# Optimization experiments

Measured on AMD Instinct MI355X. Metric: run time of the kernel, lower is better.

## Reference

```python
import jax, jax.numpy as jnp
import numpy as np

B, T, IN, H, G, O, D = 64, 256, 256, 1024, 256, 64, 4
GO = G + O  # graph_size + out_channels = 320


def _lstm_cell(x, h, c, Wih, Whh, bih, bhh):
    # torch.nn.LSTMCell gate order: i, f, g, o
    g = x @ Wih.T + h @ Whh.T + (bih + bhh)
    i, f, gg, o = jnp.split(g, 4, axis=-1)
    c_new = jax.nn.sigmoid(f) * c + jax.nn.sigmoid(i) * jnp.tanh(gg)
    h_new = jax.nn.sigmoid(o) * jnp.tanh(c_new)
    return h_new, c_new


def _mlp(x, W1, b1, W2, b2, W3, b3):
    # make_mlp with linear_depth=3: Linear->SiLU->Linear->SiLU->Linear
    x = jax.nn.silu(x @ W1.T + b1)
    x = jax.nn.silu(x @ W2.T + b2)
    return x @ W3.T + b3


def setup_inputs() -> dict:
    key = jax.random.key(0)
    ks = iter(jax.random.split(key, 64))
    def p(shape, s=0.05):
        return jax.random.normal(next(ks), shape, jnp.float32) * s
    inp = {}
    inp["z"] = jax.random.normal(next(ks), (B, IN), jnp.float32)
    inp["m_true"] = jax.random.normal(next(ks), (B, T, GO), jnp.float32)
    for pre, od in (("eh", H), ("ec", H), ("ex", O)):
        inp[pre + "_W1"] = p((H, IN)); inp[pre + "_b1"] = p((H,))
        inp[pre + "_W2"] = p((H, H));  inp[pre + "_b2"] = p((H,))
        inp[pre + "_W3"] = p((od, H)); inp[pre + "_b3"] = p((od,))
    inp["in_Wih"] = p((4 * H, GO)); inp["in_Whh"] = p((4 * H, H))
    inp["in_bih"] = p((4 * H,));    inp["in_bhh"] = p((4 * H,))
    inp["rnns_Wih"] = p((D, 4 * H, H)); inp["rnns_Whh"] = p((D, 4 * H, H))
    inp["rnns_bih"] = p((D, 4 * H));    inp["rnns_bhh"] = p((D, 4 * H))
    inp["hA_W"] = p((D, H, H)); inp["hA_b"] = p((D, H))
    inp["cA_W"] = p((D, H, H)); inp["cA_b"] = p((D, H))
    inp["lastH_W"] = p((GO, H)); inp["lastH_b"] = p((GO,))
    inp["lastC_W"] = p((GO, H)); inp["lastC_b"] = p((GO,))
    inp["out_Wih"] = p((4 * GO, H)); inp["out_Whh"] = p((4 * GO, GO))
    inp["out_bih"] = p((4 * GO,));   inp["out_bhh"] = p((4 * GO,))
    return inp


def reference(z, m_true,
              eh_W1, eh_b1, eh_W2, eh_b2, eh_W3, eh_b3,
              ec_W1, ec_b1, ec_W2, ec_b2, ec_W3, ec_b3,
              ex_W1, ex_b1, ex_W2, ex_b2, ex_W3, ex_b3,
              in_Wih, in_Whh, in_bih, in_bhh,
              rnns_Wih, rnns_Whh, rnns_bih, rnns_bhh,
              hA_W, hA_b, cA_W, cA_b,
              lastH_W, lastH_b, lastC_W, lastC_b,
              out_Wih, out_Whh, out_bih, out_bhh):
    h0 = _mlp(z, eh_W1, eh_b1, eh_W2, eh_b2, eh_W3, eh_b3)
    c0 = _mlp(z, ec_W1, ec_b1, ec_W2, ec_b2, ec_W3, ec_b3)
    x_last = _mlp(z, ex_W1, ex_b1, ex_W2, ex_b2, ex_W3, ex_b3)
    m_hat0 = jnp.concatenate(
        [jnp.zeros((z.shape[0], G), z.dtype), x_last], axis=-1)  # [B, GO]
    # flip time, use first T-1 steps; time-major for scan: [T-1, B, GO]
    mt = jnp.flip(m_true, axis=1)[:, :-1, :].transpose(1, 0, 2)

    def step(carry, m_t):
        h0_, c0_ = carry
        h2, c2 = _lstm_cell(m_t, h0_, c0_, in_Wih, in_Whh, in_bih, in_bhh)
        c1 = c2
        for i in range(D):  # recurrent_depth inner chain (fixed, structural)
            h1 = h2 @ hA_W[i].T + hA_b[i]
            c1 = c2 @ cA_W[i].T + cA_b[i]
            h2, c2 = _lstm_cell(h2, h1, c1,
                                rnns_Wih[i], rnns_Whh[i],
                                rnns_bih[i], rnns_bhh[i])
        # note: original reuses c1 (last adapter output) for last_c_adapter
        hh = h2 @ lastH_W.T + lastH_b
        cc = c1 @ lastC_W.T + lastC_b
        ho, _ = _lstm_cell(h2, hh, cc, out_Wih, out_Whh, out_bih, out_bhh)
        return (h2, c2), ho

    _, outs = jax.lax.scan(step, (h0, c0), mt)  # outs: [T-1, B, GO]
    m_hat = jnp.concatenate([m_hat0[:, None, :], outs.transpose(1, 0, 2)],
                            axis=1)  # [B, T, GO]
    return m_hat
```

## Files before the change

### kernel.cpp

```cpp
#include <hip/hip_runtime.h>


typedef unsigned int u32;
typedef unsigned long long u64;
typedef unsigned short u16;
typedef __attribute__((ext_vector_type(8))) __bf16 bf16x8;
typedef __attribute__((ext_vector_type(4))) float f32x4;

#define DEVI __device__ __forceinline__

union FRAG { bf16x8 v; u16 s[8]; u64 q[2]; };
union P4 { u64 q; u16 s[4]; };
union F4 { u64 q[2]; float f[4]; };

DEVI u16 f2bf(float x){ u32 u = __float_as_uint(x); return (u16)((u + 0x7fffu + ((u>>16)&1u)) >> 16); }
DEVI float sigm(float x){ return 1.0f/(1.0f + __expf(-x)); }
DEVI float tanh_(float x){ return 2.0f/(1.0f + __expf(-2.0f*x)) - 1.0f; }
DEVI void ast(void* p, u64 v){ __hip_atomic_store((u64*)p, v, __ATOMIC_RELAXED, __HIP_MEMORY_SCOPE_AGENT); }

#define MFMA16(a,b,c) __builtin_amdgcn_mfma_f32_16x16x32_bf16(a, b, c, 0, 0, 0)

#define NARR 168
#define NWG 169
#define NREP 21
#define NEPOCH 1276

#define SCHEDB() __builtin_amdgcn_sched_barrier(0)
#define WAITV(n) do{ SCHEDB(); \
  asm volatile("s_waitcnt vmcnt(" #n ")" ::: "memory"); \
  SCHEDB(); }while(0)

#if __has_builtin(__builtin_amdgcn_fence)
#define FENCE_ACQ() __builtin_amdgcn_fence(__ATOMIC_ACQUIRE, "agent")
#else
#define FENCE_ACQ() __hip_atomic_fence(__ATOMIC_ACQUIRE, __HIP_MEMORY_SCOPE_AGENT)
#endif

__global__ __launch_bounds__(256, 1) void k_scan(
    const float* __restrict__ m_true,
    const u16* __restrict__ Wcell, const u16* __restrict__ Win_h,
    const u16* __restrict__ Win_x, const u16* __restrict__ Wout,
    const u16* __restrict__ WccA,
    const float* __restrict__ b_in, const float* __restrict__ b_cell,
    const float* __restrict__ cAb, const float* __restrict__ b_out,
    const float* __restrict__ b_cc,
    u16* hS, u16* cS, float* cF, float* ccB, float* outp, u32* bar)
{
  const int wg = blockIdx.x;
  const int tid = threadIdx.x;
  const int wave = tid >> 6, lane = tid & 63;

  if (wg == NARR){
    if (wave == 0){
      u32* arr = bar;
      u32* go  = bar + NARR*32;
      for (u32 ep = 1; ep <= NEPOCH; ++ep){
        for(;;){
          int ok = 1;
          if (lane < 56){
            u32 a0 = __hip_atomic_load(arr + lane*32,       __ATOMIC_RELAXED, __HIP_MEMORY_SCOPE_AGENT);
            u32 a1 = __hip_atomic_load(arr + (lane+56)*32,  __ATOMIC_RELAXED, __HIP_MEMORY_SCOPE_AGENT);
            u32 a2 = __hip_atomic_load(arr + (lane+112)*32, __ATOMIC_RELAXED, __HIP_MEMORY_SCOPE_AGENT);
            ok = (a0 >= ep) && (a1 >= ep) && (a2 >= ep);
          }
          if (__all(ok)) break;
          __builtin_amdgcn_s_sleep(1);
        }
        if (lane < NREP)
          __hip_atomic_store(go + lane*32, ep, __ATOMIC_RELAXED, __HIP_MEMORY_SCOPE_AGENT);
      }
    }
    return;
  }

  int pipe, lw;
  if (wg < 160){ pipe = (wg >> 3) & 1; lw = ((wg >> 4) << 3) | (wg & 7); }
  else         { pipe = (wg - 160) >> 2; lw = 80 + ((wg - 160) & 3); }

  const int bl = lane & 15, kg = lane >> 4;
  const int pair = wave >> 1;
  const int bt = (pipe << 1) + (wave & 1);
  const int b  = (bt << 4) + bl;
  const int swz = (bl & 7) << 4;
  const int foff = ((bl << 2) + kg) << 4;
  const int woff = (bt << 15) + ((lw >> 1) << 10) + (bl << 6) + ((lw & 1) << 5) + (kg << 3);
  __shared__ __align__(16) u16 ldsW[81920];

  auto stage1 = [&](const u16* src, u16* lb, int segs){
    const u16* g = src + (lane << 3);
    u16* l = lb;
    for (int s = 0; s < segs; ++s){
      __builtin_amdgcn_global_load_lds(
          (const __attribute__((address_space(1))) void*)g,
          (__attribute__((address_space(3))) void*)l, 16, 0, 0);
      g += 512; l += 512;
    }
    SCHEDB();
  };
  auto afL = [&](const u16* lb, int row, int kb) -> bf16x8 {
    return *(const bf16x8*)((const char*)lb + row*512 + (kb ^ swz));
  };

  auto gsync = [&](u32 ep, const u16* pfsrc, int cstride, int spw, const u16* xsrc){
    SCHEDB();
    __syncthreads();
    if (tid == 0)
      __hip_atomic_store(bar + wg*32, ep, __ATOMIC_RELAXED, __HIP_MEMORY_SCOPE_AGENT);
    if (wave == 0) FENCE_ACQ();
    SCHEDB();
    if (pfsrc) stage1(pfsrc + (size_t)wave*cstride, ldsW + wave*cstride, spw);
    if (xsrc)  stage1(xsrc + wave*4096, ldsW + 65536 + wave*4096, 8);
    SCHEDB();
    if (tid == 0){
      const u32* gp = bar + NARR*32 + (wg % NREP)*32;
      while (__hip_atomic_load(gp, __ATOMIC_RELAXED, __HIP_MEMORY_SCOPE_AGENT) < ep)
        __builtin_amdgcn_s_sleep(1);
      asm volatile("" ::: "memory");
    }
    __syncthreads();
    SCHEDB();
  };

  auto phase_incell = [&](int t, const u16* hIn, u16* hOut, u16* cOut){
    f32x4 A0={0,0,0,0}, A1={0,0,0,0}, A2={0,0,0,0}, A3={0,0,0,0};
    const char* hf = (const char*)hIn + (bt << 15) + foff;
    const int ksb = pair << 4;
    int jl = (kg << 2), jj = (lw << 4) + jl;
    FRAG sh[2][8], xf[10], pa[8];
    f32x4 bg0, bg1, bg2, bg3, cpv;
    #pragma unroll
    for (int ks = 0; ks < 8; ++ks) sh[0][ks].v = *(const bf16x8*)(hf + (ksb + ks)*1024);
    #pragma unroll
    for (int ks = 0; ks < 8; ++ks) sh[1][ks].v = *(const bf16x8*)(hf + (ksb + 8 + ks)*1024);
    SCHEDB();
    if (wave < 2){
      bg0 = *(const f32x4*)(b_in +        jj);
      bg1 = *(const f32x4*)(b_in + 1024 + jj);
      bg2 = *(const f32x4*)(b_in + 2048 + jj);
      bg3 = *(const f32x4*)(b_in + 3072 + jj);
      cpv = *(const f32x4*)((const char*)cF + ((size_t)b << 12) + (jj << 2));
    } else {
      const float* xr = m_true + (size_t)b*81920 + (size_t)(255 - t)*320;
      #pragma unroll
      for (int ks = 0; ks < 10; ++ks){
        int k = (ks << 5) + (kg << 3);
        f32x4 x0 = *(const f32x4*)(xr + k);
        f32x4 x1 = *(const f32x4*)(xr + k + 4);
        xf[ks].s[0]=f2bf(x0[0]); xf[ks].s[1]=f2bf(x0[1]); xf[ks].s[2]=f2bf(x0[2]); xf[ks].s[3]=f2bf(x0[3]);
        xf[ks].s[4]=f2bf(x1[0]); xf[ks].s[5]=f2bf(x1[1]); xf[ks].s[6]=f2bf(x1[2]); xf[ks].s[7]=f2bf(x1[3]);
      }
      const char* p2 = (const char*)(Win_x + (size_t)lw*20480 + 16384);
      #pragma unroll
      for (int k2 = 0; k2 < 2; ++k2)
        #pragma unroll
        for (int rb = 0; rb < 4; ++rb)
          pa[k2*4+rb].v = *(const bf16x8*)(p2 + (rb*16 + bl)*128 + (((k2<<6)+(kg<<4)) ^ swz));
    }
    SCHEDB();
    WAITV(8);
    const u16* lbA = ldsW + (pair*2)*16384;
    #pragma unroll
    for (int ks = 0; ks < 8; ++ks){
      int kb = (ks << 6) + (kg << 4);
      FRAG a;
      a.v = afL(lbA, bl, kb);      A0 = MFMA16(a.v, sh[0][ks].v, A0);
      a.v = afL(lbA, 16 + bl, kb); A1 = MFMA16(a.v, sh[0][ks].v, A1);
      a.v = afL(lbA, 32 + bl, kb); A2 = MFMA16(a.v, sh[0][ks].v, A2);
      a.v = afL(lbA, 48 + bl, kb); A3 = MFMA16(a.v, sh[0][ks].v, A3);
    }
    WAITV(0);
    const u16* lbB = ldsW + (pair*2+1)*16384;
    #pragma unroll
    for (int ks = 0; ks < 8; ++ks){
      int kb = (ks << 6) + (kg << 4);
      FRAG a;
      a.v = afL(lbB, bl, kb);      A0 = MFMA16(a.v, sh[1][ks].v, A0);
      a.v = afL(lbB, 16 + bl, kb); A1 = MFMA16(a.v, sh[1][ks].v, A1);
      a.v = afL(lbB, 32 + bl, kb); A2 = MFMA16(a.v, sh[1][ks].v, A2);
      a.v = afL(lbB, 48 + bl, kb); A3 = MFMA16(a.v, sh[1][ks].v, A3);
    }
    if (wave >= 2){
      const u16* lb4 = ldsW + 65536;
      #pragma unroll
      for (int ks = 0; ks < 8; ++ks){
        int kb = (ks << 6) + (kg << 4);
        FRAG a;
        a.v = afL(lb4, bl, kb);      A0 = MFMA16(a.v, xf[ks].v, A0);
        a.v = afL(lb4, 16 + bl, kb); A1 = MFMA16(a.v, xf[ks].v, A1);
        a.v = afL(lb4, 32 + bl, kb); A2 = MFMA16(a.v, xf[ks].v, A2);
        a.v = afL(lb4, 48 + bl, kb); A3 = MFMA16(a.v, xf[ks].v, A3);
      }
      #pragma unroll
      for (int k2 = 0; k2 < 2; ++k2){
        A0 = MFMA16(pa[k2*4+0].v, xf[8+k2].v, A0);
        A1 = MFMA16(pa[k2*4+1].v, xf[8+k2].v, A1);
        A2 = MFMA16(pa[k2*4+2].v, xf[8+k2].v, A2);
        A3 = MFMA16(pa[k2*4+3].v, xf[8+k2].v, A3);
      }
    }
    __syncthreads();
    float* red = (float*)ldsW;
    if (wave >= 2){
      float* r = red + ((wave&1)*64 + lane)*20;
      *(f32x4*)(r+0) = A0; *(f32x4*)(r+4) = A1;
      *(f32x4*)(r+8) = A2; *(f32x4*)(r+12) = A3;
    }
    __syncthreads();
    if (wave < 2){
      const float* r = red + ((wave&1)*64 + lane)*20;
      A0 += *(const f32x4*)(r+0); A1 += *(const f32x4*)(r+4);
      A2 += *(const f32x4*)(r+8); A3 += *(const f32x4*)(r+12);
      P4 hw, cw;
      #pragma unroll
      for (int rr = 0; rr < 4; ++rr){
        float gi = A0[rr] + bg0[rr];
        float gf = A1[rr] + bg1[rr];
        float gg = A2[rr] + bg2[rr];
        float go = A3[rr] + bg3[rr];
        float cn = sigm(gf)*cpv[rr] + sigm(gi)*tanh_(gg);
        hw.s[rr] = f2bf(sigm(go)*tanh_(cn));
        cw.s[rr] = f2bf(cn);
      }
      ast((char*)hOut + woff, hw.q);
      ast((char*)cOut + woff, cw.q);
    }
  };

  auto phase_cell = [&](int i, const u16* hIn, const u16* cIn, u16* hOut, u16* cOut, bool last){
    f32x4 A0={0,0,0,0}, A1={0,0,0,0}, A2={0,0,0,0}, A3={0,0,0,0}, A4={0,0,0,0};
    const char* hf  = (const char*)hIn + (bt << 15) + foff;
    const char* cfr = (const char*)cIn + (bt << 15) + foff;
    const int ksb = pair << 4;
    int jl = (kg << 2), jj = (lw << 4) + jl;
    FRAG sh[2][8], sc[2][8];
    f32x4 bg0, bg1, bg2, bg3, bca;
    #pragma unroll
    for (int ks = 0; ks < 8; ++ks){
      sh[0][ks].v = *(const bf16x8*)(hf  + (ksb + ks)*1024);
      sc[0][ks].v = *(const bf16x8*)(cfr + (ksb + ks)*1024);
    }
    #pragma unroll
    for (int ks = 0; ks < 8; ++ks){
      sh[1][ks].v = *(const bf16x8*)(hf  + (ksb + 8 + ks)*1024);
      sc[1][ks].v = *(const bf16x8*)(cfr + (ksb + 8 + ks)*1024);
    }
    SCHEDB();
    if (wave < 2){
      bg0 = *(const f32x4*)(b_cell + i*4096 +        jj);
      bg1 = *(const f32x4*)(b_cell + i*4096 + 1024 + jj);
      bg2 = *(const f32x4*)(b_cell + i*4096 + 2048 + jj);
      bg3 = *(const f32x4*)(b_cell + i*4096 + 3072 + jj);
      bca = *(const f32x4*)(cAb + i*1024 + jj);
    }
    SCHEDB();
    WAITV(16);
    const u16* lbA = ldsW + (pair*2)*20480;
    #pragma unroll
    for (int ks = 0; ks < 8; ++ks){
      int kb = (ks << 6) + (kg << 4);
      FRAG a;
      a.v = afL(lbA, bl, kb);      A0 = MFMA16(a.v, sh[0][ks].v, A0);
      a.v = afL(lbA, 16 + bl, kb); A1 = MFMA16(a.v, sh[0][ks].v, A1);
      a.v = afL(lbA, 32 + bl, kb); A2 = MFMA16(a.v, sh[0][ks].v, A2);
      a.v = afL(lbA, 48 + bl, kb); A3 = MFMA16(a.v, sh[0][ks].v, A3);
      a.v = afL(lbA, 64 + bl, kb); A4 = MFMA16(a.v, sc[0][ks].v, A4);
    }
    WAITV(0);
    const u16* lbB = ldsW + (pair*2+1)*20480;
    #pragma unroll
    for (int ks = 0; ks < 8; ++ks){
      int kb = (ks << 6) + (kg << 4);
      FRAG a;
      a.v = afL(lbB, bl, kb);      A0 = MFMA16(a.v, sh[1][ks].v, A0);
      a.v = afL(lbB, 16 + bl, kb); A1 = MFMA16(a.v, sh[1][ks].v, A1);
      a.v = afL(lbB, 32 + bl, kb); A2 = MFMA16(a.v, sh[1][ks].v, A2);
      a.v = afL(lbB, 48 + bl, kb); A3 = MFMA16(a.v, sh[1][ks].v, A3);
      a.v = afL(lbB, 64 + bl, kb); A4 = MFMA16(a.v, sc[1][ks].v, A4);
    }
    __syncthreads();
    float* red = (float*)ldsW;
    if (wave >= 2){
      float* r = red + ((wave&1)*64 + lane)*20;
      *(f32x4*)(r+0) = A0; *(f32x4*)(r+4) = A1;
      *(f32x4*)(r+8) = A2; *(f32x4*)(r+12) = A3; *(f32x4*)(r+16) = A4;
    }
    __syncthreads();
    if (wave < 2){
      const float* r = red + ((wave&1)*64 + lane)*20;
      A0 += *(const f32x4*)(r+0); A1 += *(const f32x4*)(r+4);
      A2 += *(const f32x4*)(r+8); A3 += *(const f32x4*)(r+12);
      A4 += *(const f32x4*)(r+16);
      P4 hw, cw; F4 cf4;
      #pragma unroll
      for (int rr = 0; rr < 4; ++rr){
        float gi = A0[rr] + bg0[rr];
        float gf = A1[rr] + bg1[rr];
        float gg = A2[rr] + bg2[rr];
        float go = A3[rr] + bg3[rr];
        float c1 = A4[rr] + bca[rr];
        float cn = sigm(gf)*c1 + sigm(gi)*tanh_(gg);
        hw.s[rr] = f2bf(sigm(go)*tanh_(cn));
        cw.s[rr] = f2bf(cn);
        cf4.f[rr] = cn;
      }
      ast((char*)hOut + woff, hw.q);
      ast((char*)cOut + woff, cw.q);
      if (last){
        char* cfp = (char*)cF + ((size_t)b << 12) + (jj << 2);
        ast(cfp, cf4.q[0]); ast(cfp + 8, cf4.q[1]);
      }
    }
  };

  auto phase_ccA = [&](const u16* cIn){
    f32x4 A = {0,0,0,0};
    int w2 = lw - 64;
    const char* cfr = (const char*)cIn + (bt << 15) + foff;
    const int ksb = pair << 4;
    int jl = (kg << 2), jjo = (w2 << 4) + jl;
    FRAG sc[2][8];
    f32x4 bcc;
    #pragma unroll
    for (int ks = 0; ks < 8; ++ks) sc[0][ks].v = *(const bf16x8*)(cfr + (ksb + ks)*1024);
    #pragma unroll
    for (int ks = 0; ks < 8; ++ks) sc[1][ks].v = *(const bf16x8*)(cfr + (ksb + 8 + ks)*1024);
    SCHEDB();
    if (wave < 2) bcc = *(const f32x4*)(b_cc + jjo);
    SCHEDB();
    WAITV(8);
    const u16* lbA = ldsW + (pair*2)*4096;
    #pragma unroll
    for (int ks = 0; ks < 8; ++ks){
      int kb = (ks << 6) + (kg << 4);
      FRAG a; a.v = afL(lbA, bl, kb);
      A = MFMA16(a.v, sc[0][ks].v, A);
    }
    WAITV(0);
    const u16* lbB = ldsW + (pair*2+1)*4096;
    #pragma unroll
    for (int ks = 0; ks < 8; ++ks){
      int kb = (ks << 6) + (kg << 4);
      FRAG a; a.v = afL(lbB, bl, kb);
      A = MFMA16(a.v, sc[1][ks].v, A);
    }
    __syncthreads();
    float* red = (float*)ldsW;
    if (wave >= 2) *(f32x4*)(red + ((wave&1)*64 + lane)*20) = A;
    __syncthreads();
    if (wave < 2){
      A += *(const f32x4*)(red + ((wave&1)*64 + lane)*20);
      F4 v;
      #pragma unroll
      for (int rr = 0; rr < 4; ++rr) v.f[rr] = A[rr] + bcc[rr];
      char* cp2 = (char*)ccB + ((size_t)b*320 + jjo)*4;
      ast(cp2, v.q[0]); ast(cp2 + 8, v.q[1]);
    }
  };

  auto phase_out = [&](int t, const u16* hIn){
    f32x4 A0={0,0,0,0}, A1={0,0,0,0}, A2={0,0,0,0}, A3={0,0,0,0};
    int w2 = lw - 64;
    const char* hf = (const char*)hIn + (bt << 15) + foff;
    const int ksb = pair << 4;
    int jl = (kg << 2), jjo = (w2 << 4) + jl;
    FRAG sh[2][8];
    f32x4 bg0, bg1, bg2, bg3, ccv;
    #pragma unroll
    for (int ks = 0; ks < 8; ++ks) sh[0][ks].v = *(const bf16x8*)(hf + (ksb + ks)*1024);
    #pragma unroll
    for (int ks = 0; ks < 8; ++ks) sh[1][ks].v = *(const bf16x8*)(hf + (ksb + 8 + ks)*1024);
    SCHEDB();
    if (wave < 2){
      bg0 = *(const f32x4*)(b_out +       jjo);
      bg1 = *(const f32x4*)(b_out + 320 + jjo);
      bg2 = *(const f32x4*)(b_out + 640 + jjo);
      bg3 = *(const f32x4*)(b_out + 960 + jjo);
      ccv = *(const f32x4*)((const char*)ccB + ((size_t)b*320 + jjo)*4);
    }
    SCHEDB();
    WAITV(8);
    const u16* lbA = ldsW + (pair*2)*16384;
    #pragma unroll
    for (int ks = 0; ks < 8; ++ks){
      int kb = (ks << 6) + (kg << 4);
      FRAG a;
      a.v = afL(lbA, bl, kb);      A0 = MFMA16(a.v, sh[0][ks].v, A0);
      a.v = afL(lbA, 16 + bl, kb); A1 = MFMA16(a.v, sh[0][ks].v, A1);
      a.v = afL(lbA, 32 + bl, kb); A2 = MFMA16(a.v, sh[0][ks].v, A2);
      a.v = afL(lbA, 48 + bl, kb); A3 = MFMA16(a.v, sh[0][ks].v, A3);
    }
    WAITV(0);
    const u16* lbB = ldsW + (pair*2+1)*16384;
    #pragma unroll
    for (int ks = 0; ks < 8; ++ks){
      int kb = (ks << 6) + (kg << 4);
      FRAG a;
      a.v = afL(lbB, bl, kb);      A0 = MFMA16(a.v, sh[1][ks].v, A0);
      a.v = afL(lbB, 16 + bl, kb); A1 = MFMA16(a.v, sh[1][ks].v, A1);
      a.v = afL(lbB, 32 + bl, kb); A2 = MFMA16(a.v, sh[1][ks].v, A2);
      a.v = afL(lbB, 48 + bl, kb); A3 = MFMA16(a.v, sh[1][ks].v, A3);
    }
    __syncthreads();
    float* red = (float*)ldsW;
    if (wave >= 2){
      float* r = red + ((wave&1)*64 + lane)*20;
      *(f32x4*)(r+0) = A0; *(f32x4*)(r+4) = A1;
      *(f32x4*)(r+8) = A2; *(f32x4*)(r+12) = A3;
    }
    __syncthreads();
    if (wave < 2){
      const float* r = red + ((wave&1)*64 + lane)*20;
      A0 += *(const f32x4*)(r+0); A1 += *(const f32x4*)(r+4);
      A2 += *(const f32x4*)(r+8); A3 += *(const f32x4*)(r+12);
      f32x4 ho;
      #pragma unroll
      for (int rr = 0; rr < 4; ++rr){
        float gi = A0[rr] + bg0[rr];
        float gf = A1[rr] + bg1[rr];
        float gg = A2[rr] + bg2[rr];
        float go = A3[rr] + bg3[rr];
        float cn = sigm(gf)*ccv[rr] + sigm(gi)*tanh_(gg);
        ho[rr] = sigm(go)*tanh_(cn);
      }
      *(f32x4*)(outp + (size_t)b*81920 + (size_t)(t+1)*320 + jjo) = ho;
    }
  };

  if (lw < 64){
    stage1(Win_h + ((size_t)lw << 16) + wave*16384, ldsW + wave*16384, 32);
    stage1(Win_x + (size_t)lw*20480 + wave*4096, ldsW + 65536 + wave*4096, 8);
  }
  __syncthreads();
  SCHEDB();

  u16* hB0 = hS;        u16* hB1 = hS + 65536;
  u16* cB0 = cS;        u16* cB1 = cS + 65536;

  u32 ep = 1;
  if (lw < 64) phase_incell(0, hB1, hB0, cB0);
  gsync(ep++, (lw < 64) ? Wcell + (size_t)lw*81920 : nullptr, 20480, 40, nullptr);
  int p = 1;
  #pragma unroll 1
  for (int t = 0; t < 255; ++t){
    #pragma unroll 1
    for (int i = 0; i < 4; ++i){
      u16* hIn = (p & 1) ? hB0 : hB1;  u16* cIn = (p & 1) ? cB0 : cB1;
      u16* hOut = (p & 1) ? hB1 : hB0; u16* cOut = (p & 1) ? cB1 : cB0;
      if (lw < 64)      phase_cell(i, hIn, cIn, hOut, cOut, i == 3);
      else if (i == 3)  phase_ccA(cIn);
      const u16* pf = nullptr; const u16* xs = nullptr; int cstride = 0, spw = 0;
      if (lw < 64){
        if (i < 3){ pf = Wcell + (size_t)((i+1)*64 + lw)*81920; cstride = 20480; spw = 40; }
        else      { pf = Win_h + ((size_t)lw << 16); cstride = 16384; spw = 32;
                    xs = Win_x + (size_t)lw*20480; }
      } else {
        if (i == 2){ pf = WccA + ((size_t)(lw-64) << 14); cstride = 4096; spw = 8; }
        else if (i == 3){ pf = Wout + ((size_t)(lw-64) << 16); cstride = 16384; spw = 32; }
      }
      gsync(ep++, pf, cstride, spw, xs);
      ++p;
    }
    u16* hIn = (p & 1) ? hB0 : hB1;
    u16* hOut = (p & 1) ? hB1 : hB0; u16* cOut = (p & 1) ? cB1 : cB0;
    if (lw >= 64)       phase_out(t, hIn);
    else if (t < 254)   phase_incell(t + 1, hIn, hOut, cOut);
    gsync(ep++, (lw < 64 && t < 254) ? Wcell + (size_t)lw*81920 : nullptr, 20480, 40, nullptr);
    ++p;
  }
}


__global__ __launch_bounds__(256) void k_dense(const float* __restrict__ X, int xmode,
    const float* __restrict__ W, const float* __restrict__ bias,
    int OD, int ID, int act, int omode, float* outF, u16* outB)
{
  int o = blockIdx.x*4 + (threadIdx.x >> 6);
  if (o >= OD) return;
  int lane = threadIdx.x & 63;
  const float* wr = W + (size_t)o*ID;
  float acc = 0.f;
  if (xmode == 0){ for (int k = 0; k < ID; ++k) acc = fmaf(wr[k], X[(size_t)lane*ID + k], acc); }
  else           { for (int k = 0; k < ID; ++k) acc = fmaf(wr[k], X[(size_t)k*64 + lane], acc); }
  acc += bias[o];
  if (act) acc = acc * sigm(acc);
  if (omode == 0)      outF[(size_t)o*64 + lane] = acc;
  else if (omode == 1){
    int bt = lane >> 4, blx = lane & 15;
    outB[(size_t)bt*16384 + (size_t)(o>>5)*512 + blx*32 + ((o&31)>>3)*8 + (o&7)] = f2bf(acc);
  }
  else if (omode == 2) outF[(size_t)lane*1024 + o] = acc;
  else                 outF[(size_t)lane*81920 + 256 + o] = acc;
}

__global__ void k_zero0(float* out){ out[(size_t)blockIdx.x*81920 + threadIdx.x] = 0.f; }

__global__ __launch_bounds__(256) void k_tr(const float* __restrict__ in, u16* __restrict__ out, int M, int N){
  __shared__ u16 t[64][65];
  int m0 = blockIdx.x << 6, n0 = blockIdx.y << 6;
  int c = threadIdx.x & 63, rq = threadIdx.x >> 6;
  for (int rr = 0; rr < 16; ++rr){
    int r = (rq << 4) + rr;
    t[r][c] = f2bf(in[(size_t)(m0 + r)*N + n0 + c]);
  }
  __syncthreads();
  for (int rr = 0; rr < 16; ++rr){
    int r = (rq << 4) + rr;
    out[(size_t)(n0 + r)*M + m0 + c] = t[c][r];
  }
}

__global__ __launch_bounds__(256) void k_fuse(const float* __restrict__ Whh, const float* __restrict__ Wih,
    const u16* __restrict__ BT, int KM, int mode, u16* __restrict__ dst)
{
  int bx = blockIdx.x, by = blockIdx.y, bz = blockIdx.z;
  int lane = threadIdx.x & 63, wv = threadIdx.x >> 6;
  int bl = lane & 15, kg = lane >> 4;
  int jbase = (mode == 0) ? bz*1024 : ((mode == 1) ? bz*320 : 0);
  int jrow = jbase + bx*16 + bl;
  int k2c = by*64 + wv*16 + bl;
  f32x4 acc = {0,0,0,0};
  for (int m0 = 0; m0 < KM; m0 += 32){
    f32x4 wa0 = *(const f32x4*)(Whh + (size_t)jrow*KM + m0 + (kg << 3));
    f32x4 wa1 = *(const f32x4*)(Whh + (size_t)jrow*KM + m0 + (kg << 3) + 4);
    FRAG a;
    a.s[0]=f2bf(wa0[0]); a.s[1]=f2bf(wa0[1]); a.s[2]=f2bf(wa0[2]); a.s[3]=f2bf(wa0[3]);
    a.s[4]=f2bf(wa1[0]); a.s[5]=f2bf(wa1[1]); a.s[6]=f2bf(wa1[2]); a.s[7]=f2bf(wa1[3]);
    FRAG bb; bb.v = *(const bf16x8*)(BT + (size_t)k2c*KM + m0 + (kg << 3));
    acc = MFMA16(a.v, bb.v, acc);
  }
  #pragma unroll
  for (int r = 0; r < 4; ++r){
    int jl = (kg << 2) + r;
    int jg = jbase + bx*16 + jl;
    float v = acc[r];
    if (mode < 2) v += Wih[(size_t)jg*1024 + k2c];
    int re = (mode == 2) ? jl : (bz*16 + jl);
    int c = k2c >> 8, kl = k2c & 255;
    size_t pos;
    if (mode == 0)      pos = (size_t)bx*81920 + c*20480 + re*256 + (kl ^ ((re&7)<<3));
    else if (mode == 1) pos = (size_t)bx*65536 + c*16384 + re*256 + (kl ^ ((re&7)<<3));
    else                pos = (size_t)bx*16384 + c*4096  + re*256 + (kl ^ ((re&7)<<3));
    dst[pos] = f2bf(v);
  }
}

__global__ void k_pack_winh(const float* __restrict__ src, u16* __restrict__ dst){
  int id = blockIdx.x*256 + threadIdx.x;
  int j = id >> 10, k = id & 1023;
  int g = j >> 10, jj = j & 1023;
  int w = jj >> 4, r = (g << 4) + (jj & 15);
  int c = k >> 8, kl = k & 255;
  dst[(size_t)w*65536 + c*16384 + r*256 + (kl ^ ((r&7)<<3))] = f2bf(src[id]);
}

__global__ void k_pack_winx(const float* __restrict__ src, u16* __restrict__ dst){
  int j = blockIdx.x, k = threadIdx.x;
  int g = j >> 10, jj = j & 1023;
  int w = jj >> 4, r = (g << 4) + (jj & 15);
  float v = src[(size_t)j*320 + k];
  size_t pos;
  if (k < 256) pos = (size_t)w*20480 + r*256 + (k ^ ((r&7)<<3));
  else         pos = (size_t)w*20480 + 16384 + r*64 + ((k - 256) ^ ((r&7)<<3));
  dst[pos] = f2bf(v);
}

__global__ void k_pack_ca(const float* __restrict__ src, u16* __restrict__ dst){
  int id = blockIdx.x*256 + threadIdx.x;
  int jj = id >> 10, k = id & 1023;
  int w = jj >> 4, r = 64 + (jj & 15);
  int c = k >> 8, kl = k & 255;
  dst[(size_t)w*81920 + c*20480 + r*256 + (kl ^ ((r&7)<<3))] = f2bf(src[id]);
}

__global__ __launch_bounds__(256) void k_bias(const float* __restrict__ A, const float* __restrict__ x,
    const float* __restrict__ a1, const float* __restrict__ a2, float* __restrict__ o, int NJ, int K)
{
  int j = blockIdx.x*4 + (threadIdx.x >> 6);
  if (j >= NJ) return;
  int lane = threadIdx.x & 63;
  float acc = 0.f;
  if (A) for (int k = lane; k < K; k += 64) acc += A[(size_t)j*K + k]*x[k];
  for (int off = 32; off; off >>= 1) acc += __shfl_down(acc, off);
  if (lane == 0) o[j] = acc + (a1 ? a1[j] : 0.f) + (a2 ? a2[j] : 0.f);
}

extern "C" void kernel_launch(void* const* d_in, const int* in_sizes, int n_in,
                              void* d_out, int out_size, void* d_ws, size_t ws_size,
                              hipStream_t stream)
{
  (void)in_sizes; (void)n_in; (void)out_size;
  const float* z      = (const float*)d_in[0];
  const float* m_true = (const float*)d_in[1];
  const float* eh_W1=(const float*)d_in[2],  *eh_b1=(const float*)d_in[3];
  const float* eh_W2=(const float*)d_in[4],  *eh_b2=(const float*)d_in[5];
  const float* eh_W3=(const float*)d_in[6],  *eh_b3=(const float*)d_in[7];
  const float* ec_W1=(const float*)d_in[8],  *ec_b1=(const float*)d_in[9];
  const float* ec_W2=(const float*)d_in[10], *ec_b2=(const float*)d_in[11];
  const float* ec_W3=(const float*)d_in[12], *ec_b3=(const float*)d_in[13];
  const float* ex_W1=(const float*)d_in[14], *ex_b1=(const float*)d_in[15];
  const float* ex_W2=(const float*)d_in[16], *ex_b2=(const float*)d_in[17];
  const float* ex_W3=(const float*)d_in[18], *ex_b3=(const float*)d_in[19];
  const float* in_Wih=(const float*)d_in[20], *in_Whh=(const float*)d_in[21];
  const float* in_bih=(const float*)d_in[22], *in_bhh=(const float*)d_in[23];
  const float* r_Wih=(const float*)d_in[24],  *r_Whh=(const float*)d_in[25];
  const float* r_bih=(const float*)d_in[26],  *r_bhh=(const float*)d_in[27];
  const float* hA_W=(const float*)d_in[28],   *hA_b=(const float*)d_in[29];
  const float* cA_W=(const float*)d_in[30],   *cA_b=(const float*)d_in[31];
  const float* lastH_W=(const float*)d_in[32], *lastH_b=(const float*)d_in[33];
  const float* lastC_W=(const float*)d_in[34], *lastC_b=(const float*)d_in[35];
  const float* out_Wih=(const float*)d_in[36], *out_Whh=(const float*)d_in[37];
  const float* out_bih=(const float*)d_in[38], *out_bhh=(const float*)d_in[39];
  float* out = (float*)d_out;

  char* wsb = (char*)d_ws;
  size_t off = 0;
  auto alloc = [&](size_t bytes)->char*{
    char* p = wsb + off; off = (off + bytes + 255) & ~(size_t)255; return p;
  };
  u32* bar    = (u32*)alloc(256*32*4);
  u16* hS     = (u16*)alloc(2*64*1024*2);
  u16* cS     = (u16*)alloc(2*64*1024*2);
  float* cF   = (float*)alloc(64*1024*4);
  float* ccB  = (float*)alloc(64*320*4);
  float* b_in = (float*)alloc(4096*4);
  float* b_cell=(float*)alloc(4*4096*4);
  float* b_out= (float*)alloc(1280*4);
  float* b_cc = (float*)alloc(320*4);
  float* t1   = (float*)alloc(1024*64*4);
  float* t2   = (float*)alloc(1024*64*4);
  u16* Tbuf   = (u16*)alloc((size_t)1024*1024*2);
  u16* Win_h  = (u16*)alloc((size_t)64*65536*2);
  u16* Win_x  = (u16*)alloc((size_t)64*20480*2);
  u16* Wcell  = (u16*)alloc((size_t)4*64*81920*2);
  u16* Wout   = (u16*)alloc((size_t)20*65536*2);
  u16* WccA   = (u16*)alloc((size_t)20*16384*2);
  if (off > ws_size) return;

  hipMemsetAsync(bar, 0, 256*32*4, stream);

  k_dense<<<256,256,0,stream>>>(z, 0, eh_W1, eh_b1, 1024, 256, 1, 0, t1, nullptr);
  k_dense<<<256,256,0,stream>>>(t1,1, eh_W2, eh_b2, 1024,1024, 1, 0, t2, nullptr);
  k_dense<<<256,256,0,stream>>>(t2,1, eh_W3, eh_b3, 1024,1024, 0, 1, nullptr, hS + 65536);
  k_dense<<<256,256,0,stream>>>(z, 0, ec_W1, ec_b1, 1024, 256, 1, 0, t1, nullptr);
  k_dense<<<256,256,0,stream>>>(t1,1, ec_W2, ec_b2, 1024,1024, 1, 0, t2, nullptr);
  k_dense<<<256,256,0,stream>>>(t2,1, ec_W3, ec_b3, 1024,1024, 0, 2, cF, nullptr);
  k_dense<<<256,256,0,stream>>>(z, 0, ex_W1, ex_b1, 1024, 256, 1, 0, t1, nullptr);
  k_dense<<<256,256,0,stream>>>(t1,1, ex_W2, ex_b2, 1024,1024, 1, 0, t2, nullptr);
  k_dense<<<16 ,256,0,stream>>>(t2,1, ex_W3, ex_b3,   64,1024, 0, 3, out, nullptr);
  k_zero0<<<64,256,0,stream>>>(out);

  k_pack_winh<<<16384,256,0,stream>>>(in_Whh, Win_h);
  k_pack_winx<<<4096,320,0,stream>>>(in_Wih, Win_x);
  for (int i = 0; i < 4; ++i)
    k_pack_ca<<<4096,256,0,stream>>>(cA_W + (size_t)i*1024*1024, Wcell + (size_t)i*64*81920);

  for (int i = 0; i < 4; ++i){
    k_tr<<<dim3(16,16),256,0,stream>>>(hA_W + (size_t)i*1024*1024, Tbuf, 1024, 1024);
    k_fuse<<<dim3(64,16,4),256,0,stream>>>(r_Whh + (size_t)i*4096*1024,
                                           r_Wih + (size_t)i*4096*1024,
                                           Tbuf, 1024, 0, Wcell + (size_t)i*64*81920);
  }
  k_tr<<<dim3(5,16),256,0,stream>>>(lastH_W, Tbuf, 320, 1024);
  k_fuse<<<dim3(20,16,4),256,0,stream>>>(out_Whh, out_Wih, Tbuf, 320, 1, Wout);
  k_tr<<<dim3(16,16),256,0,stream>>>(cA_W + (size_t)3*1024*1024, Tbuf, 1024, 1024);
  k_fuse<<<dim3(20,16,1),256,0,stream>>>(lastC_W, nullptr, Tbuf, 1024, 2, WccA);

  k_bias<<<1024,256,0,stream>>>(nullptr, nullptr, in_bih, in_bhh, b_in, 4096, 0);
  for (int i = 0; i < 4; ++i)
    k_bias<<<1024,256,0,stream>>>(r_Whh + (size_t)i*4096*1024, hA_b + i*1024,
                                  r_bih + i*4096, r_bhh + i*4096, b_cell + i*4096, 4096, 1024);
  k_bias<<<320,256,0,stream>>>(out_Whh, lastH_b, out_bih, out_bhh, b_out, 1280, 320);
  k_bias<<<80 ,256,0,stream>>>(lastC_W, cA_b + 3*1024, lastC_b, nullptr, b_cc, 320, 1024);

  k_scan<<<NWG,256,0,stream>>>(m_true, Wcell, Win_h, Win_x, Wout, WccA,
                               b_in, b_cell, cA_b, b_out, b_cc,
                               hS, cS, cF, ccB, out, bar);
}
```

Before: 12.20 ms.

## Replace arbiter-block barrier with per-pipe flag polling and keep cell state in registers

Removes the dedicated arbiter workgroup that gathered arrival flags and broadcast go signals. Each workgroup's wave 0 now polls the arrival flags of its own pipe (84 workgroups) directly, which cuts one hop from every grid barrier. The final cell state and the ccA adapter output are kept in registers across steps instead of round-tripping through global buffers. Loads are issued through inline asm with sc0/sc1 cache-bypass bits and finer vmcnt waits so more memory traffic overlaps the MFMAs. Correctness now depends on the relaxed flag polling plus the cache-bypass loads giving enough memory ordering without an explicit acquire fence.

```diff
diff --git a/kernel.cpp b/kernel.cpp
--- a/kernel.cpp
+++ b/kernel.cpp
@@ -18,23 +18,24 @@
 DEVI float tanh_(float x){ return 2.0f/(1.0f + __expf(-2.0f*x)) - 1.0f; }
 DEVI void ast(void* p, u64 v){ __hip_atomic_store((u64*)p, v, __ATOMIC_RELAXED, __HIP_MEMORY_SCOPE_AGENT); }
 
+DEVI void ld16sc(FRAG& d, const void* p){
+  asm volatile("global_load_dwordx4 %0, %1, off sc0 sc1" : "=v"(d.v) : "v"(p));
+}
+DEVI void ld16(FRAG& d, const void* p){
+  asm volatile("global_load_dwordx4 %0, %1, off" : "=v"(d.v) : "v"(p));
+}
+DEVI void ldf4(f32x4& d, const void* p){
+  asm volatile("global_load_dwordx4 %0, %1, off" : "=v"(d) : "v"(p));
+}
+
 #define MFMA16(a,b,c) __builtin_amdgcn_mfma_f32_16x16x32_bf16(a, b, c, 0, 0, 0)
 
-#define NARR 168
-#define NWG 169
-#define NREP 21
-#define NEPOCH 1276
+#define NWG 168
 
 #define SCHEDB() __builtin_amdgcn_sched_barrier(0)
 #define WAITV(n) do{ SCHEDB(); \
   asm volatile("s_waitcnt vmcnt(" #n ")" ::: "memory"); \
   SCHEDB(); }while(0)
-
-#if __has_builtin(__builtin_amdgcn_fence)
-#define FENCE_ACQ() __builtin_amdgcn_fence(__ATOMIC_ACQUIRE, "agent")
-#else
-#define FENCE_ACQ() __hip_atomic_fence(__ATOMIC_ACQUIRE, __HIP_MEMORY_SCOPE_AGENT)
-#endif
 
 __global__ __launch_bounds__(256, 1) void k_scan(
     const float* __restrict__ m_true,
@@ -44,34 +45,11 @@
     const float* __restrict__ b_in, const float* __restrict__ b_cell,
     const float* __restrict__ cAb, const float* __restrict__ b_out,
     const float* __restrict__ b_cc,
-    u16* hS, u16* cS, float* cF, float* ccB, float* outp, u32* bar)
+    u16* hS, u16* cS, float* cF, float* outp, u32* bar)
 {
   const int wg = blockIdx.x;
   const int tid = threadIdx.x;
   const int wave = tid >> 6, lane = tid & 63;
-
-  if (wg == NARR){
-    if (wave == 0){
-      u32* arr = bar;
-      u32* go  = bar + NARR*32;
-      for (u32 ep = 1; ep <= NEPOCH; ++ep){
-        for(;;){
-          int ok = 1;
-          if (lane < 56){
-            u32 a0 = __hip_atomic_load(arr + lane*32,       __ATOMIC_RELAXED, __HIP_MEMORY_SCOPE_AGENT);
-            u32 a1 = __hip_atomic_load(arr + (lane+56)*32,  __ATOMIC_RELAXED, __HIP_MEMORY_SCOPE_AGENT);
-            u32 a2 = __hip_atomic_load(arr + (lane+112)*32, __ATOMIC_RELAXED, __HIP_MEMORY_SCOPE_AGENT);
-            ok = (a0 >= ep) && (a1 >= ep) && (a2 >= ep);
-          }
-          if (__all(ok)) break;
-          __builtin_amdgcn_s_sleep(1);
-        }
-        if (lane < NREP)
-          __hip_atomic_store(go + lane*32, ep, __ATOMIC_RELAXED, __HIP_MEMORY_SCOPE_AGENT);
-      }
-    }
-    return;
-  }
 
   int pipe, lw;
   if (wg < 160){ pipe = (wg >> 3) & 1; lw = ((wg >> 4) << 3) | (wg & 7); }
@@ -84,7 +62,13 @@
   const int swz = (bl & 7) << 4;
   const int foff = ((bl << 2) + kg) << 4;
   const int woff = (bt << 15) + ((lw >> 1) << 10) + (bl << 6) + ((lw & 1) << 5) + (kg << 3);
+  u32* flagp = bar + (pipe*128 + lw)*32;
+  const u32* fbase = bar + pipe*128*32;
+  const int i2 = (lane < 20) ? 64 + lane : lane;
   __shared__ __align__(16) u16 ldsW[81920];
+
+  f32x4 cprev = {0,0,0,0};
+  f32x4 ccreg = {0,0,0,0};
 
   auto stage1 = [&](const u16* src, u16* lb, int segs){
     const u16* g = src + (lane << 3);
@@ -105,17 +89,18 @@
     SCHEDB();
     __syncthreads();
     if (tid == 0)
-      __hip_atomic_store(bar + wg*32, ep, __ATOMIC_RELAXED, __HIP_MEMORY_SCOPE_AGENT);
-    if (wave == 0) FENCE_ACQ();
+      __hip_atomic_store(flagp, ep, __ATOMIC_RELAXED, __HIP_MEMORY_SCOPE_AGENT);
     SCHEDB();
     if (pfsrc) stage1(pfsrc + (size_t)wave*cstride, ldsW + wave*cstride, spw);
     if (xsrc)  stage1(xsrc + wave*4096, ldsW + 65536 + wave*4096, 8);
     SCHEDB();
-    if (tid == 0){
-      const u32* gp = bar + NARR*32 + (wg % NREP)*32;
-      while (__hip_atomic_load(gp, __ATOMIC_RELAXED, __HIP_MEMORY_SCOPE_AGENT) < ep)
+    if (wave == 0){
+      for(;;){
+        u32 a = __hip_atomic_load(fbase + lane*32, __ATOMIC_RELAXED, __HIP_MEMORY_SCOPE_AGENT);
+        u32 c2 = __hip_atomic_load(fbase + i2*32, __ATOMIC_RELAXED, __HIP_MEMORY_SCOPE_AGENT);
+        if (__all(a >= ep && c2 >= ep)) break;
         __builtin_amdgcn_s_sleep(1);
-      asm volatile("" ::: "memory");
+      }
     }
     __syncthreads();
     SCHEDB();
@@ -126,20 +111,49 @@
     const char* hf = (const char*)hIn + (bt << 15) + foff;
     const int ksb = pair << 4;
     int jl = (kg << 2), jj = (lw << 4) + jl;
-    FRAG sh[2][8], xf[10], pa[8];
-    f32x4 bg0, bg1, bg2, bg3, cpv;
-    #pragma unroll
-    for (int ks = 0; ks < 8; ++ks) sh[0][ks].v = *(const bf16x8*)(hf + (ksb + ks)*1024);
-    #pragma unroll
-    for (int ks = 0; ks < 8; ++ks) sh[1][ks].v = *(const bf16x8*)(hf + (ksb + 8 + ks)*1024);
-    SCHEDB();
-    if (wave < 2){
-      bg0 = *(const f32x4*)(b_in +        jj);
-      bg1 = *(const f32x4*)(b_in + 1024 + jj);
-      bg2 = *(const f32x4*)(b_in + 2048 + jj);
-      bg3 = *(const f32x4*)(b_in + 3072 + jj);
-      cpv = *(const f32x4*)((const char*)cF + ((size_t)b << 12) + (jj << 2));
-    } else {
+    FRAG sh[2][8], pa[8];
+    f32x4 bg0, bg1, bg2, bg3;
+    #pragma unroll
+    for (int ks = 0; ks < 8; ++ks) ld16sc(sh[0][ks], hf + (ksb + ks)*1024);
+    #pragma unroll
+    for (int ks = 0; ks < 8; ++ks) ld16sc(sh[1][ks], hf + (ksb + 8 + ks)*1024);
+    {
+      const char* p2 = (const char*)(Win_x + (size_t)lw*20480 + 16384);
+      #pragma unroll
+      for (int k2 = 0; k2 < 2; ++k2)
+        #pragma unroll
+        for (int rb = 0; rb < 4; ++rb)
+          ld16(pa[k2*4+rb], p2 + (rb*16 + bl)*128 + (((k2<<6)+(kg<<4)) ^ swz));
+    }
+    ldf4(bg0, b_in +        jj);
+    ldf4(bg1, b_in + 1024 + jj);
+    ldf4(bg2, b_in + 2048 + jj);
+    ldf4(bg3, b_in + 3072 + jj);
+    WAITV(20);
+    const u16* lbA = ldsW + (pair*2)*16384;
+    #pragma unroll
+    for (int ks = 0; ks < 8; ++ks){
+      int kb = (ks << 6) + (kg << 4);
+      FRAG a;
+      a.v = afL(lbA, bl, kb);      A0 = MFMA16(a.v, sh[0][ks].v, A0);
+      a.v = afL(lbA, 16 + bl, kb); A1 = MFMA16(a.v, sh[0][ks].v, A1);
+      a.v = afL(lbA, 32 + bl, kb); A2 = MFMA16(a.v, sh[0][ks].v, A2);
+      a.v = afL(lbA, 48 + bl, kb); A3 = MFMA16(a.v, sh[0][ks].v, A3);
+    }
+    WAITV(12);
+    const u16* lbB = ldsW + (pair*2+1)*16384;
+    #pragma unroll
+    for (int ks = 0; ks < 8; ++ks){
+      int kb = (ks << 6) + (kg << 4);
+      FRAG a;
+      a.v = afL(lbB, bl, kb);      A0 = MFMA16(a.v, sh[1][ks].v, A0);
+      a.v = afL(lbB, 16 + bl, kb); A1 = MFMA16(a.v, sh[1][ks].v, A1);
+      a.v = afL(lbB, 32 + bl, kb); A2 = MFMA16(a.v, sh[1][ks].v, A2);
+      a.v = afL(lbB, 48 + bl, kb); A3 = MFMA16(a.v, sh[1][ks].v, A3);
+    }
+    WAITV(4);
+    if (wave >= 2){
+      FRAG xf[10];
       const float* xr = m_true + (size_t)b*81920 + (size_t)(255 - t)*320;
       #pragma unroll
       for (int ks = 0; ks < 10; ++ks){
@@ -149,37 +163,6 @@
         xf[ks].s[0]=f2bf(x0[0]); xf[ks].s[1]=f2bf(x0[1]); xf[ks].s[2]=f2bf(x0[2]); xf[ks].s[3]=f2bf(x0[3]);
         xf[ks].s[4]=f2bf(x1[0]); xf[ks].s[5]=f2bf(x1[1]); xf[ks].s[6]=f2bf(x1[2]); xf[ks].s[7]=f2bf(x1[3]);
       }
-      const char* p2 = (const char*)(Win_x + (size_t)lw*20480 + 16384);
-      #pragma unroll
-      for (int k2 = 0; k2 < 2; ++k2)
-        #pragma unroll
-        for (int rb = 0; rb < 4; ++rb)
-          pa[k2*4+rb].v = *(const bf16x8*)(p2 + (rb*16 + bl)*128 + (((k2<<6)+(kg<<4)) ^ swz));
-    }
-    SCHEDB();
-    WAITV(8);
-    const u16* lbA = ldsW + (pair*2)*16384;
-    #pragma unroll
-    for (int ks = 0; ks < 8; ++ks){
-      int kb = (ks << 6) + (kg << 4);
-      FRAG a;
-      a.v = afL(lbA, bl, kb);      A0 = MFMA16(a.v, sh[0][ks].v, A0);
-      a.v = afL(lbA, 16 + bl, kb); A1 = MFMA16(a.v, sh[0][ks].v, A1);
-      a.v = afL(lbA, 32 + bl, kb); A2 = MFMA16(a.v, sh[0][ks].v, A2);
-      a.v = afL(lbA, 48 + bl, kb); A3 = MFMA16(a.v, sh[0][ks].v, A3);
-    }
-    WAITV(0);
-    const u16* lbB = ldsW + (pair*2+1)*16384;
-    #pragma unroll
-    for (int ks = 0; ks < 8; ++ks){
-      int kb = (ks << 6) + (kg << 4);
-      FRAG a;
-      a.v = afL(lbB, bl, kb);      A0 = MFMA16(a.v, sh[1][ks].v, A0);
-      a.v = afL(lbB, 16 + bl, kb); A1 = MFMA16(a.v, sh[1][ks].v, A1);
-      a.v = afL(lbB, 32 + bl, kb); A2 = MFMA16(a.v, sh[1][ks].v, A2);
-      a.v = afL(lbB, 48 + bl, kb); A3 = MFMA16(a.v, sh[1][ks].v, A3);
-    }
-    if (wave >= 2){
       const u16* lb4 = ldsW + 65536;
       #pragma unroll
       for (int ks = 0; ks < 8; ++ks){
@@ -217,7 +200,7 @@
         float gf = A1[rr] + bg1[rr];
         float gg = A2[rr] + bg2[rr];
         float go = A3[rr] + bg3[rr];
-        float cn = sigm(gf)*cpv[rr] + sigm(gi)*tanh_(gg);
+        float cn = sigm(gf)*cprev[rr] + sigm(gi)*tanh_(gg);
         hw.s[rr] = f2bf(sigm(go)*tanh_(cn));
         cw.s[rr] = f2bf(cn);
       }
@@ -235,25 +218,19 @@
     FRAG sh[2][8], sc[2][8];
     f32x4 bg0, bg1, bg2, bg3, bca;
     #pragma unroll
-    for (int ks = 0; ks < 8; ++ks){
-      sh[0][ks].v = *(const bf16x8*)(hf  + (ksb + ks)*1024);
-      sc[0][ks].v = *(const bf16x8*)(cfr + (ksb + ks)*1024);
-    }
-    #pragma unroll
-    for (int ks = 0; ks < 8; ++ks){
-      sh[1][ks].v = *(const bf16x8*)(hf  + (ksb + 8 + ks)*1024);
-      sc[1][ks].v = *(const bf16x8*)(cfr + (ksb + 8 + ks)*1024);
-    }
-    SCHEDB();
-    if (wave < 2){
-      bg0 = *(const f32x4*)(b_cell + i*4096 +        jj);
-      bg1 = *(const f32x4*)(b_cell + i*4096 + 1024 + jj);
-      bg2 = *(const f32x4*)(b_cell + i*4096 + 2048 + jj);
-      bg3 = *(const f32x4*)(b_cell + i*4096 + 3072 + jj);
-      bca = *(const f32x4*)(cAb + i*1024 + jj);
-    }
-    SCHEDB();
-    WAITV(16);
+    for (int ks = 0; ks < 8; ++ks) ld16sc(sh[0][ks], hf  + (ksb + ks)*1024);
+    #pragma unroll
+    for (int ks = 0; ks < 8; ++ks) ld16sc(sc[0][ks], cfr + (ksb + ks)*1024);
+    #pragma unroll
+    for (int ks = 0; ks < 8; ++ks) ld16sc(sh[1][ks], hf  + (ksb + 8 + ks)*1024);
+    #pragma unroll
+    for (int ks = 0; ks < 8; ++ks) ld16sc(sc[1][ks], cfr + (ksb + 8 + ks)*1024);
+    ldf4(bg0, b_cell + i*4096 +        jj);
+    ldf4(bg1, b_cell + i*4096 + 1024 + jj);
+    ldf4(bg2, b_cell + i*4096 + 2048 + jj);
+    ldf4(bg3, b_cell + i*4096 + 3072 + jj);
+    ldf4(bca, cAb + i*1024 + jj);
+    WAITV(21);
     const u16* lbA = ldsW + (pair*2)*20480;
     #pragma unroll
     for (int ks = 0; ks < 8; ++ks){
@@ -265,7 +242,7 @@
       a.v = afL(lbA, 48 + bl, kb); A3 = MFMA16(a.v, sh[0][ks].v, A3);
       a.v = afL(lbA, 64 + bl, kb); A4 = MFMA16(a.v, sc[0][ks].v, A4);
     }
-    WAITV(0);
+    WAITV(5);
     const u16* lbB = ldsW + (pair*2+1)*20480;
     #pragma unroll
     for (int ks = 0; ks < 8; ++ks){
@@ -305,29 +282,23 @@
       }
       ast((char*)hOut + woff, hw.q);
       ast((char*)cOut + woff, cw.q);
-      if (last){
-        char* cfp = (char*)cF + ((size_t)b << 12) + (jj << 2);
-        ast(cfp, cf4.q[0]); ast(cfp + 8, cf4.q[1]);
-      }
+      if (last){ cprev[0]=cf4.f[0]; cprev[1]=cf4.f[1]; cprev[2]=cf4.f[2]; cprev[3]=cf4.f[3]; }
     }
   };
 
   auto phase_ccA = [&](const u16* cIn){
     f32x4 A = {0,0,0,0};
-    int w2 = lw - 64;
     const char* cfr = (const char*)cIn + (bt << 15) + foff;
     const int ksb = pair << 4;
-    int jl = (kg << 2), jjo = (w2 << 4) + jl;
+    int jl = (kg << 2), jjo = ((lw - 64) << 4) + jl;
     FRAG sc[2][8];
     f32x4 bcc;
     #pragma unroll
-    for (int ks = 0; ks < 8; ++ks) sc[0][ks].v = *(const bf16x8*)(cfr + (ksb + ks)*1024);
-    #pragma unroll
-    for (int ks = 0; ks < 8; ++ks) sc[1][ks].v = *(const bf16x8*)(cfr + (ksb + 8 + ks)*1024);
-    SCHEDB();
-    if (wave < 2) bcc = *(const f32x4*)(b_cc + jjo);
-    SCHEDB();
-    WAITV(8);
+    for (int ks = 0; ks < 8; ++ks) ld16sc(sc[0][ks], cfr + (ksb + ks)*1024);
+    #pragma unroll
+    for (int ks = 0; ks < 8; ++ks) ld16sc(sc[1][ks], cfr + (ksb + 8 + ks)*1024);
+    ldf4(bcc, b_cc + jjo);
+    WAITV(9);
     const u16* lbA = ldsW + (pair*2)*4096;
     #pragma unroll
     for (int ks = 0; ks < 8; ++ks){
@@ -335,7 +306,7 @@
       FRAG a; a.v = afL(lbA, bl, kb);
       A = MFMA16(a.v, sc[0][ks].v, A);
     }
-    WAITV(0);
+    WAITV(1);
     const u16* lbB = ldsW + (pair*2+1)*4096;
     #pragma unroll
     for (int ks = 0; ks < 8; ++ks){
@@ -349,36 +320,27 @@
     __syncthreads();
     if (wave < 2){
       A += *(const f32x4*)(red + ((wave&1)*64 + lane)*20);
-      F4 v;
-      #pragma unroll
-      for (int rr = 0; rr < 4; ++rr) v.f[rr] = A[rr] + bcc[rr];
-      char* cp2 = (char*)ccB + ((size_t)b*320 + jjo)*4;
-      ast(cp2, v.q[0]); ast(cp2 + 8, v.q[1]);
+      #pragma unroll
+      for (int rr = 0; rr < 4; ++rr) ccreg[rr] = A[rr] + bcc[rr];
     }
   };
 
   auto phase_out = [&](int t, const u16* hIn){
     f32x4 A0={0,0,0,0}, A1={0,0,0,0}, A2={0,0,0,0}, A3={0,0,0,0};
-    int w2 = lw - 64;
     const char* hf = (const char*)hIn + (bt << 15) + foff;
     const int ksb = pair << 4;
-    int jl = (kg << 2), jjo = (w2 << 4) + jl;
+    int jl = (kg << 2), jjo = ((lw - 64) << 4) + jl;
     FRAG sh[2][8];
-    f32x4 bg0, bg1, bg2, bg3, ccv;
-    #pragma unroll
-    for (int ks = 0; ks < 8; ++ks) sh[0][ks].v = *(const bf16x8*)(hf + (ksb + ks)*1024);
-    #pragma unroll
-    for (int ks = 0; ks < 8; ++ks) sh[1][ks].v = *(const bf16x8*)(hf + (ksb + 8 + ks)*1024);
-    SCHEDB();
-    if (wave < 2){
-      bg0 = *(const f32x4*)(b_out +       jjo);
-      bg1 = *(const f32x4*)(b_out + 320 + jjo);
-      bg2 = *(const f32x4*)(b_out + 640 + jjo);
-      bg3 = *(const f32x4*)(b_out + 960 + jjo);
-      ccv = *(const f32x4*)((const char*)ccB + ((size_t)b*320 + jjo)*4);
-    }
-    SCHEDB();
-    WAITV(8);
+    f32x4 bg0, bg1, bg2, bg3;
+    #pragma unroll
+    for (int ks = 0; ks < 8; ++ks) ld16sc(sh[0][ks], hf + (ksb + ks)*1024);
+    #pragma unroll
+    for (int ks = 0; ks < 8; ++ks) ld16sc(sh[1][ks], hf + (ksb + 8 + ks)*1024);
+    ldf4(bg0, b_out +       jjo);
+    ldf4(bg1, b_out + 320 + jjo);
+    ldf4(bg2, b_out + 640 + jjo);
+    ldf4(bg3, b_out + 960 + jjo);
+    WAITV(12);
     const u16* lbA = ldsW + (pair*2)*16384;
     #pragma unroll
     for (int ks = 0; ks < 8; ++ks){
@@ -389,7 +351,7 @@
       a.v = afL(lbA, 32 + bl, kb); A2 = MFMA16(a.v, sh[0][ks].v, A2);
       a.v = afL(lbA, 48 + bl, kb); A3 = MFMA16(a.v, sh[0][ks].v, A3);
     }
-    WAITV(0);
+    WAITV(4);
     const u16* lbB = ldsW + (pair*2+1)*16384;
     #pragma unroll
     for (int ks = 0; ks < 8; ++ks){
@@ -419,7 +381,7 @@
         float gf = A1[rr] + bg1[rr];
         float gg = A2[rr] + bg2[rr];
         float go = A3[rr] + bg3[rr];
-        float cn = sigm(gf)*ccv[rr] + sigm(gi)*tanh_(gg);
+        float cn = sigm(gf)*ccreg[rr] + sigm(gi)*tanh_(gg);
         ho[rr] = sigm(go)*tanh_(cn);
       }
       *(f32x4*)(outp + (size_t)b*81920 + (size_t)(t+1)*320 + jjo) = ho;
@@ -427,6 +389,10 @@
   };
 
   if (lw < 64){
+    if (wave < 2){
+      int jj = (lw << 4) + (kg << 2);
+      cprev = *(const f32x4*)(cF + (size_t)b*1024 + jj);
+    }
     stage1(Win_h + ((size_t)lw << 16) + wave*16384, ldsW + wave*16384, 32);
     stage1(Win_x + (size_t)lw*20480 + wave*4096, ldsW + 65536 + wave*4096, 8);
   }
@@ -621,7 +587,6 @@
   u16* hS     = (u16*)alloc(2*64*1024*2);
   u16* cS     = (u16*)alloc(2*64*1024*2);
   float* cF   = (float*)alloc(64*1024*4);
-  float* ccB  = (float*)alloc(64*320*4);
   float* b_in = (float*)alloc(4096*4);
   float* b_cell=(float*)alloc(4*4096*4);
   float* b_out= (float*)alloc(1280*4);
@@ -674,5 +639,5 @@
 
   k_scan<<<NWG,256,0,stream>>>(m_true, Wcell, Win_h, Win_x, Wout, WccA,
                                b_in, b_cell, cA_b, b_out, b_cc,
-                               hS, cS, cF, ccB, out, bar);
-}
+                               hS, cS, cF, out, bar);
+}
```

Result: faster. 11.81 ms (-3.2%).
